# Kernel optimization log

Hardware: AMD Instinct MI355X
Metric: run time of the kernel (lower is better)

The kernel has to match this reference:

```python
import jax, jax.numpy as jnp
import numpy as np

C = 256          # channels
G = 4            # dcn groups
GC = C // G      # channels per group
K = 3            # dcn kernel size
P = K * K        # sampling points per group
OS = 0.5         # offset_scale
PAD = 1
N, H, W = 2, 128, 128


def setup_inputs() -> dict:
    key = jax.random.key(0)
    ks = jax.random.split(key, 8)
    f = lambda k, shp, s: jax.random.normal(k, shp, dtype=jnp.float32) * s
    return {
        "sampled_feat": jax.random.normal(ks[0], (N, H, W, C), dtype=jnp.float32),
        "context_info": jax.random.normal(ks[1], (N, H, W, C), dtype=jnp.float32),
        "W_in": f(ks[2], (C, C), 0.02),            # input_proj weight
        "b_in": jnp.zeros((C,), jnp.float32),
        "dw_kernel": f(ks[3], (3, 3, 1, C), 0.02),  # depthwise conv (HWIO, I=1)
        "dw_bias": jnp.zeros((C,), jnp.float32),
        "W_om": f(ks[4], (C, G * P * 3), 0.01),     # offset+mask projection
        "b_om": jnp.zeros((G * P * 3,), jnp.float32),
        "W_out": f(ks[5], (C, C), 0.02),            # output_proj (no bias)
        "ln_gamma": jnp.ones((C,), jnp.float32),
        "ln_beta": jnp.zeros((C,), jnp.float32),
    }


def _dcn_forward(sampled_feat, context_info, W_in, b_in, dw_kernel, dw_bias,
                 W_om, b_om, W_out, ln_gamma, ln_beta):
    Hp, Wp = H + 2 * PAD, W + 2 * PAD
    # value branch: pointwise input_proj then spatial zero-pad
    value = sampled_feat @ W_in + b_in
    value = jnp.pad(value, ((0, 0), (PAD, PAD), (PAD, PAD), (0, 0)))
    valg = value.reshape(N, Hp * Wp, G, GC).transpose(0, 2, 1, 3)  # (N,G,Hp*Wp,GC)

    # offset/mask branch (extra_offset_mask=True -> computed from context_info)
    ctx = jax.lax.conv_general_dilated(
        context_info, dw_kernel, (1, 1), ((1, 1), (1, 1)),
        dimension_numbers=("NHWC", "HWIO", "NHWC"), feature_group_count=C) + dw_bias
    om = (ctx @ W_om + b_om).reshape(N, H, W, G, 3 * P)
    offset = om[..., :2 * P].reshape(N, H, W, G, P, 2)  # (x,y) per sampling point
    mask = om[..., 2 * P:]                               # (N,H,W,G,P); DCNv4: no softmax

    # sampling locations in padded-input pixel coords (align_corners=False convention)
    kk = jnp.arange(K, dtype=jnp.float32) - (K - 1) // 2
    kx = jnp.tile(kk, K)      # (P,)
    ky = jnp.repeat(kk, K)    # (P,)
    base_x = (jnp.arange(W, dtype=jnp.float32) + PAD)[None, None, :, None, None]
    base_y = (jnp.arange(H, dtype=jnp.float32) + PAD)[None, :, None, None, None]
    px = base_x + OS * (kx + offset[..., 0])   # (N,H,W,G,P)
    py = base_y + OS * (ky + offset[..., 1])
    px = px.transpose(0, 3, 1, 2, 4).reshape(N, G, -1)  # (N,G,H*W*P)
    py = py.transpose(0, 3, 1, 2, 4).reshape(N, G, -1)

    # bilinear sampling with zero padding outside the padded input
    x0 = jnp.floor(px); y0 = jnp.floor(py)
    wx1 = px - x0; wy1 = py - y0

    def corner(xi, yi, w):
        valid = (xi >= 0) & (xi <= Wp - 1) & (yi >= 0) & (yi <= Hp - 1)
        idx = (jnp.clip(yi, 0, Hp - 1) * Wp + jnp.clip(xi, 0, Wp - 1)).astype(jnp.int32)
        v = jnp.take_along_axis(valg, idx[..., None], axis=2)  # (N,G,S,GC)
        return v * (w * valid)[..., None]

    samp = (corner(x0, y0, (1 - wx1) * (1 - wy1))
            + corner(x0 + 1, y0, wx1 * (1 - wy1))
            + corner(x0, y0 + 1, (1 - wx1) * wy1)
            + corner(x0 + 1, y0 + 1, wx1 * wy1))
    samp = samp.reshape(N, G, H, W, P, GC)
    maskg = mask.transpose(0, 3, 1, 2, 4)  # (N,G,H,W,P)
    out = jnp.einsum("nghwpc,nghwp->nhwgc", samp, maskg).reshape(N, H, W, C)

    out = out @ W_out  # output_proj, output_bias=False
    # LayerNorm over channels + exact GELU
    mu = out.mean(-1, keepdims=True)
    var = out.var(-1, keepdims=True)
    out = (out - mu) * jax.lax.rsqrt(var + 1e-5) * ln_gamma + ln_beta
    return jax.nn.gelu(out, approximate=False)


def reference(sampled_feat, context_info, W_in, b_in, dw_kernel, dw_bias,
              W_om, b_om, W_out, ln_gamma, ln_beta):
    return _dcn_forward(sampled_feat, context_info, W_in, b_in, dw_kernel, dw_bias,
                        W_om, b_om, W_out, ln_gamma, ln_beta)
```

## Files before the change

### kernel.cpp

```cpp
#include <hip/hip_runtime.h>
#include <math.h>

constexpr int NBATCH = 2, HH = 128, WW = 128, CC = 256, GC = 64;
constexpr int PP = 9, OMW = 108;
constexpr int MM = NBATCH * HH * WW;
constexpr int BTCOLS = 640;

using bf8 = __attribute__((ext_vector_type(8))) short;
using f32x4 = __attribute__((ext_vector_type(4))) float;

__device__ __forceinline__ short f2bf(float x) {
  unsigned u = __builtin_bit_cast(unsigned, x);
  unsigned r = (u + 0x7fffu + ((u >> 16) & 1u)) >> 16;
  return (short)r;
}
__device__ __forceinline__ float bf2f(short h) {
  unsigned u = ((unsigned)(unsigned short)h) << 16;
  return __builtin_bit_cast(float, u);
}

__global__ __launch_bounds__(256) void prep_kernel(
    const float* __restrict__ Win, const float* __restrict__ Wom,
    const float* __restrict__ Wout, short* __restrict__ Bh,
    short* __restrict__ Bl) {
  int gid = blockIdx.x * 256 + threadIdx.x;
  int col = gid >> 8, k = gid & 255;
  float w;
  if (col < 256)
    w = Win[k * 256 + col];
  else if (col < 384) {
    int c = col - 256;
    w = (c < OMW) ? Wom[k * OMW + c] : 0.f;
  } else {
    int c = col - 384;
    w = Wout[k * 256 + c];
  }
  short h = f2bf(w);
  short l = f2bf(w - bf2f(h));
  Bh[gid] = h;
  Bl[gid] = l;
}

__global__ __launch_bounds__(256) void dwconv_kernel(
    const float* __restrict__ x, const float* __restrict__ k,
    const float* __restrict__ b, float* __restrict__ y) {
  int gid = blockIdx.x * 256 + threadIdx.x;
  int q = gid & 63;
  int m = gid >> 6;
  int c = q * 4;
  int w = m & 127, h = (m >> 7) & 127, n = m >> 14;
  float4 acc = *(const float4*)&b[c];
#pragma unroll
  for (int dy = 0; dy < 3; ++dy) {
    int yy = h + dy - 1;
    if (yy < 0 || yy >= HH) continue;
#pragma unroll
    for (int dx = 0; dx < 3; ++dx) {
      int xx = w + dx - 1;
      if (xx < 0 || xx >= WW) continue;
      float4 v = *(const float4*)&x[(((size_t)n * HH + yy) * WW + xx) * CC + c];
      float4 kk = *(const float4*)&k[(dy * 3 + dx) * CC + c];
      acc.x += v.x * kk.x;
      acc.y += v.y * kk.y;
      acc.z += v.z * kk.z;
      acc.w += v.w * kk.w;
    }
  }
  *(float4*)&y[(size_t)m * CC + c] = acc;
}

template <int BN, int NOUT, bool BIAS, bool LN>
__global__ __launch_bounds__(BN == 256 ? 512 : 256) void mgemm(
    const float* __restrict__ A, const short* __restrict__ Bth,
    const short* __restrict__ Btl, const float* __restrict__ bias,
    float* __restrict__ Co, const float* __restrict__ lng,
    const float* __restrict__ lnb) {
  constexpr int BM = 128, BK = 32;
  constexpr int NT = (BN == 256) ? 512 : 256;
  constexpr int WN = BN / 64;
  __shared__ __align__(16) short Ah[BM][BK], Al[BM][BK];
  __shared__ __align__(16) short Bh[BN][BK], Bl[BN][BK];
  const int t = threadIdx.x;
  const int lane = t & 63, wid = t >> 6;
  const int wr = wid / WN, wc = wid % WN;
  const int l15 = lane & 15, l4 = lane >> 4;
  int mb, nb;
  if constexpr (BN == 128 && NOUT == 256) {
    mb = (int)(blockIdx.x >> 1) * BM;
    nb = (int)(blockIdx.x & 1) * 128;
  } else {
    mb = (int)blockIdx.x * BM;
    nb = 0;
  }

  f32x4 acc[4][4];
#pragma unroll
  for (int r = 0; r < 4; ++r)
#pragma unroll
    for (int n = 0; n < 4; ++n) acc[r][n] = (f32x4){0.f, 0.f, 0.f, 0.f};

  for (int ks = 0; ks < 256; ks += BK) {
#pragma unroll
    for (int i = 0; i < (BM * BK / 4) / NT; ++i) {
      int idx = t + NT * i;
      int row = idx >> 3, kq = idx & 7;
      float4 v = *(const float4*)&A[(size_t)(mb + row) * 256 + ks + kq * 4];
      short4 h = make_short4(f2bf(v.x), f2bf(v.y), f2bf(v.z), f2bf(v.w));
      short4 l =
          make_short4(f2bf(v.x - bf2f(h.x)), f2bf(v.y - bf2f(h.y)),
                      f2bf(v.z - bf2f(h.z)), f2bf(v.w - bf2f(h.w)));
      *(short4*)&Ah[row][kq * 4] = h;
      *(short4*)&Al[row][kq * 4] = l;
    }
#pragma unroll
    for (int i = 0; i < (BN * 4) / NT; ++i) {
      int idx = t + NT * i;
      int col = idx >> 2, q = idx & 3;
      *(bf8*)&Bh[col][q * 8] =
          *(const bf8*)&Bth[(size_t)(nb + col) * 256 + ks + q * 8];
      *(bf8*)&Bl[col][q * 8] =
          *(const bf8*)&Btl[(size_t)(nb + col) * 256 + ks + q * 8];
    }
    __syncthreads();

    bf8 ah[4], al[4], bh[4], bl[4];
#pragma unroll
    for (int r = 0; r < 4; ++r) {
      int row = wr * 64 + r * 16 + l15;
      ah[r] = *(const bf8*)&Ah[row][l4 * 8];
      al[r] = *(const bf8*)&Al[row][l4 * 8];
    }
#pragma unroll
    for (int n = 0; n < 4; ++n) {
      int col = wc * 64 + n * 16 + l15;
      bh[n] = *(const bf8*)&Bh[col][l4 * 8];
      bl[n] = *(const bf8*)&Bl[col][l4 * 8];
    }
#pragma unroll
    for (int r = 0; r < 4; ++r)
#pragma unroll
      for (int n = 0; n < 4; ++n) {
        acc[r][n] =
            __builtin_amdgcn_mfma_f32_16x16x32_bf16(al[r], bh[n], acc[r][n], 0, 0, 0);
        acc[r][n] =
            __builtin_amdgcn_mfma_f32_16x16x32_bf16(ah[r], bl[n], acc[r][n], 0, 0, 0);
        acc[r][n] =
            __builtin_amdgcn_mfma_f32_16x16x32_bf16(ah[r], bh[n], acc[r][n], 0, 0, 0);
      }
    __syncthreads();
  }

  if constexpr (LN) {
    __shared__ float red[BM][2];
    __shared__ float mu_s[BM], rs_s[BM];
    if (t < BM) {
      red[t][0] = 0.f;
      red[t][1] = 0.f;
    }
    __syncthreads();
#pragma unroll
    for (int r = 0; r < 4; ++r) {
#pragma unroll
      for (int reg = 0; reg < 4; ++reg) {
        float s = 0.f, ss = 0.f;
#pragma unroll
        for (int n = 0; n < 4; ++n) {
          float v = acc[r][n][reg];
          s += v;
          ss += v * v;
        }
#pragma unroll
        for (int m = 1; m < 16; m <<= 1) {
          s += __shfl_xor(s, m);
          ss += __shfl_xor(ss, m);
        }
        if (l15 == 0) {
          int row = wr * 64 + r * 16 + l4 * 4 + reg;
          atomicAdd(&red[row][0], s);
          atomicAdd(&red[row][1], ss);
        }
      }
    }
    __syncthreads();
    if (t < BM) {
      float mu = red[t][0] * (1.f / 256.f);
      float var = red[t][1] * (1.f / 256.f) - mu * mu;
      mu_s[t] = mu;
      rs_s[t] = rsqrtf(var + 1e-5f);
    }
    __syncthreads();
#pragma unroll
    for (int r = 0; r < 4; ++r)
#pragma unroll
      for (int reg = 0; reg < 4; ++reg) {
        int rloc = wr * 64 + r * 16 + l4 * 4 + reg;
        int row = mb + rloc;
        float mu = mu_s[rloc], rs = rs_s[rloc];
#pragma unroll
        for (int n = 0; n < 4; ++n) {
          int col = nb + wc * 64 + n * 16 + l15;
          float v = (acc[r][n][reg] - mu) * rs * lng[col] + lnb[col];
          Co[(size_t)row * NOUT + col] =
              0.5f * v * (1.f + erff(v * 0.70710678118654752f));
        }
      }
  } else {
#pragma unroll
    for (int r = 0; r < 4; ++r)
#pragma unroll
      for (int reg = 0; reg < 4; ++reg) {
        int row = mb + wr * 64 + r * 16 + l4 * 4 + reg;
#pragma unroll
        for (int n = 0; n < 4; ++n) {
          int col = nb + wc * 64 + n * 16 + l15;
          if (NOUT == BN * (256 / BN) || col < NOUT) {
            float v = acc[r][n][reg];
            if constexpr (BIAS) v += bias[col];
            if (col < NOUT) Co[(size_t)row * NOUT + col] = v;
          }
        }
      }
  }
}

__global__ __launch_bounds__(256) void sample_kernel(
    const float* __restrict__ val, const float* __restrict__ om,
    float* __restrict__ out) {
  int gid = blockIdx.x * 256 + threadIdx.x;
  int q = gid & 63;
  int m = gid >> 6;
  int g = q >> 4;
  int w = m & 127, h = (m >> 7) & 127, n = m >> 14;
  const float* omp = om + m * OMW + g * 27;
  const float* vb = val + (n << 22) + (q << 2);
  float bx = (float)(w + 1), by = (float)(h + 1);
  float4 acc = make_float4(0.f, 0.f, 0.f, 0.f);

#pragma unroll
  for (int p = 0; p < PP; ++p) {
    float px = bx + 0.5f * ((float)(p % 3 - 1) + omp[2 * p]);
    float py = by + 0.5f * ((float)(p / 3 - 1) + omp[2 * p + 1]);
    float mk = omp[18 + p];
    float x0f = floorf(px), y0f = floorf(py);
    int x0 = (int)x0f, y0 = (int)y0f;
    float wx1 = px - x0f, wy1 = py - y0f;
    float wx0 = 1.f - wx1, wy0 = 1.f - wy1;
    float4 s = make_float4(0.f, 0.f, 0.f, 0.f);
#define CORNER(XC, YC, WT)                                            \
  {                                                                   \
    int xc = (XC), yc = (YC);                                         \
    int xi = min(max(xc, 1), 128), yi = min(max(yc, 1), 128);         \
    float wt = ((xc == xi) && (yc == yi)) ? (WT) : 0.f;               \
    const float4 v =                                                  \
        *(const float4*)&vb[(((yi - 1) << 7) + (xi - 1)) << 8];       \
    s.x += v.x * wt;                                                  \
    s.y += v.y * wt;                                                  \
    s.z += v.z * wt;                                                  \
    s.w += v.w * wt;                                                  \
  }
    CORNER(x0, y0, wx0 * wy0);
    CORNER(x0 + 1, y0, wx1 * wy0);
    CORNER(x0, y0 + 1, wx0 * wy1);
    CORNER(x0 + 1, y0 + 1, wx1 * wy1);
#undef CORNER
    acc.x += mk * s.x;
    acc.y += mk * s.y;
    acc.z += mk * s.z;
    acc.w += mk * s.w;
  }
  *(float4*)&out[((size_t)m << 8) + (q << 2)] = acc;
}

extern "C" void kernel_launch(void* const* d_in, const int* in_sizes, int n_in,
                              void* d_out, int out_size, void* d_ws,
                              size_t ws_size, hipStream_t stream) {
  (void)in_sizes;
  (void)n_in;
  (void)out_size;
  (void)ws_size;
  const float* sampled = (const float*)d_in[0];
  const float* ctxin = (const float*)d_in[1];
  const float* W_in = (const float*)d_in[2];
  const float* b_in = (const float*)d_in[3];
  const float* dwk = (const float*)d_in[4];
  const float* dwb = (const float*)d_in[5];
  const float* W_om = (const float*)d_in[6];
  const float* b_om = (const float*)d_in[7];
  const float* W_out = (const float*)d_in[8];
  const float* lng = (const float*)d_in[9];
  const float* lnb = (const float*)d_in[10];
  float* out = (float*)d_out;

  float* ws = (float*)d_ws;
  float* value = ws;
  float* omb = value + (size_t)MM * CC;
  float* ctx_dcn = omb + (size_t)MM * OMW;
  short* Bth = (short*)(ctx_dcn + (size_t)MM * CC);
  short* Btl = Bth + (size_t)BTCOLS * 256;

  prep_kernel<<<BTCOLS, 256, 0, stream>>>(W_in, W_om, W_out, Bth, Btl);
  dwconv_kernel<<<MM * 64 / 256, 256, 0, stream>>>(ctxin, dwk, dwb, ctx_dcn);
  mgemm<128, 108, true, false><<<MM / 128, 256, 0, stream>>>(
      ctx_dcn, Bth + 256 * 256, Btl + 256 * 256, b_om, omb, nullptr, nullptr);
  mgemm<128, 256, true, false><<<2 * (MM / 128), 256, 0, stream>>>(
      sampled, Bth, Btl, b_in, value, nullptr, nullptr);
  sample_kernel<<<MM * 64 / 256, 256, 0, stream>>>(value, omb, ctx_dcn);
  mgemm<256, 256, false, true><<<MM / 128, 512, 0, stream>>>(
      ctx_dcn, Bth + 384 * 256, Btl + 384 * 256, nullptr, out, lng, lnb);
}
```

Measured before the change: 248.6 us.

## Pre-split activations to bf16 hi/lo and retile GEMMs with separate LN-GELU pass

Producers (dwconv, sample, and a new split kernel for the input features) now write bf16 hi/lo pairs directly, so the GEMM no longer converts fp32 A tiles inside its loop. The GEMM is retiled to 64x128 blocks with BK=64, padded shared-memory rows and an occupancy hint, and one kernel serves all three projections. The fused LayerNorm+GELU epilogue moves into a separate row-wise kernel, which adds an extra fp32 round trip through memory and two more launches.

Result: slower. 266.1 us (+7.1%).

```diff
diff --git a/kernel.cpp b/kernel.cpp
--- a/kernel.cpp
+++ b/kernel.cpp
@@ -1,7 +1,7 @@
 #include <hip/hip_runtime.h>
 #include <math.h>
 
-constexpr int NBATCH = 2, HH = 128, WW = 128, CC = 256, GC = 64;
+constexpr int NBATCH = 2, HH = 128, WW = 128, CC = 256;
 constexpr int PP = 9, OMW = 108;
 constexpr int MM = NBATCH * HH * WW;
 constexpr int BTCOLS = 640;
@@ -17,6 +17,12 @@
 __device__ __forceinline__ float bf2f(short h) {
   unsigned u = ((unsigned)(unsigned short)h) << 16;
   return __builtin_bit_cast(float, u);
+}
+__device__ __forceinline__ void split4(float4 v, short4* h, short4* l) {
+  short4 hh = make_short4(f2bf(v.x), f2bf(v.y), f2bf(v.z), f2bf(v.w));
+  *h = hh;
+  *l = make_short4(f2bf(v.x - bf2f(hh.x)), f2bf(v.y - bf2f(hh.y)),
+                   f2bf(v.z - bf2f(hh.z)), f2bf(v.w - bf2f(hh.w)));
 }
 
 __global__ __launch_bounds__(256) void prep_kernel(
@@ -36,14 +42,25 @@
     w = Wout[k * 256 + c];
   }
   short h = f2bf(w);
-  short l = f2bf(w - bf2f(h));
   Bh[gid] = h;
-  Bl[gid] = l;
+  Bl[gid] = f2bf(w - bf2f(h));
+}
+
+__global__ __launch_bounds__(256) void split_kernel(
+    const float* __restrict__ x, short* __restrict__ h,
+    short* __restrict__ l) {
+  int gid = blockIdx.x * 256 + threadIdx.x;
+  float4 v = *(const float4*)&x[(size_t)gid * 4];
+  short4 hh, ll;
+  split4(v, &hh, &ll);
+  *(short4*)&h[(size_t)gid * 4] = hh;
+  *(short4*)&l[(size_t)gid * 4] = ll;
 }
 
 __global__ __launch_bounds__(256) void dwconv_kernel(
     const float* __restrict__ x, const float* __restrict__ k,
-    const float* __restrict__ b, float* __restrict__ y) {
+    const float* __restrict__ b, short* __restrict__ yh,
+    short* __restrict__ yl) {
   int gid = blockIdx.x * 256 + threadIdx.x;
   int q = gid & 63;
   int m = gid >> 6;
@@ -66,166 +83,103 @@
       acc.w += v.w * kk.w;
     }
   }
-  *(float4*)&y[(size_t)m * CC + c] = acc;
-}
-
-template <int BN, int NOUT, bool BIAS, bool LN>
-__global__ __launch_bounds__(BN == 256 ? 512 : 256) void mgemm(
-    const float* __restrict__ A, const short* __restrict__ Bth,
-    const short* __restrict__ Btl, const float* __restrict__ bias,
-    float* __restrict__ Co, const float* __restrict__ lng,
-    const float* __restrict__ lnb) {
-  constexpr int BM = 128, BK = 32;
-  constexpr int NT = (BN == 256) ? 512 : 256;
-  constexpr int WN = BN / 64;
-  __shared__ __align__(16) short Ah[BM][BK], Al[BM][BK];
-  __shared__ __align__(16) short Bh[BN][BK], Bl[BN][BK];
+  short4 hh, ll;
+  split4(acc, &hh, &ll);
+  *(short4*)&yh[(size_t)m * CC + c] = hh;
+  *(short4*)&yl[(size_t)m * CC + c] = ll;
+}
+
+template <bool GUARD, bool BIAS>
+__global__ __launch_bounds__(256, 3) void mgemm(
+    const short* __restrict__ Ath, const short* __restrict__ Atl,
+    const short* __restrict__ Bth, const short* __restrict__ Btl,
+    const float* __restrict__ bias, float* __restrict__ Co, int nshift,
+    int nout) {
+  constexpr int BM = 64, BN = 128, BK = 64, SK = 68;
+  __shared__ __align__(16) short As[2][BM * SK];
+  __shared__ __align__(16) short Bs[2][BN * SK];
   const int t = threadIdx.x;
   const int lane = t & 63, wid = t >> 6;
-  const int wr = wid / WN, wc = wid % WN;
+  const int wr = wid >> 1, wc = wid & 1;
   const int l15 = lane & 15, l4 = lane >> 4;
-  int mb, nb;
-  if constexpr (BN == 128 && NOUT == 256) {
-    mb = (int)(blockIdx.x >> 1) * BM;
-    nb = (int)(blockIdx.x & 1) * 128;
-  } else {
-    mb = (int)blockIdx.x * BM;
-    nb = 0;
-  }
-
-  f32x4 acc[4][4];
-#pragma unroll
-  for (int r = 0; r < 4; ++r)
+  const int mb = ((int)blockIdx.x >> nshift) * BM;
+  const int nb = ((int)blockIdx.x & ((1 << nshift) - 1)) * BN;
+
+  f32x4 acc[2][4];
+#pragma unroll
+  for (int r = 0; r < 2; ++r)
 #pragma unroll
     for (int n = 0; n < 4; ++n) acc[r][n] = (f32x4){0.f, 0.f, 0.f, 0.f};
 
   for (int ks = 0; ks < 256; ks += BK) {
 #pragma unroll
-    for (int i = 0; i < (BM * BK / 4) / NT; ++i) {
-      int idx = t + NT * i;
-      int row = idx >> 3, kq = idx & 7;
-      float4 v = *(const float4*)&A[(size_t)(mb + row) * 256 + ks + kq * 4];
-      short4 h = make_short4(f2bf(v.x), f2bf(v.y), f2bf(v.z), f2bf(v.w));
-      short4 l =
-          make_short4(f2bf(v.x - bf2f(h.x)), f2bf(v.y - bf2f(h.y)),
-                      f2bf(v.z - bf2f(h.z)), f2bf(v.w - bf2f(h.w)));
-      *(short4*)&Ah[row][kq * 4] = h;
-      *(short4*)&Al[row][kq * 4] = l;
-    }
-#pragma unroll
-    for (int i = 0; i < (BN * 4) / NT; ++i) {
-      int idx = t + NT * i;
-      int col = idx >> 2, q = idx & 3;
-      *(bf8*)&Bh[col][q * 8] =
-          *(const bf8*)&Bth[(size_t)(nb + col) * 256 + ks + q * 8];
-      *(bf8*)&Bl[col][q * 8] =
-          *(const bf8*)&Btl[(size_t)(nb + col) * 256 + ks + q * 8];
+    for (int i = 0; i < 2; ++i) {
+      int idx = t + 256 * i;
+      int row = idx >> 3, kq = (idx & 7) * 8;
+      size_t g = (size_t)(mb + row) * 256 + ks + kq;
+      *(bf8*)&As[0][row * SK + kq] = *(const bf8*)&Ath[g];
+      *(bf8*)&As[1][row * SK + kq] = *(const bf8*)&Atl[g];
+    }
+#pragma unroll
+    for (int i = 0; i < 4; ++i) {
+      int idx = t + 256 * i;
+      int col = idx >> 3, kq = (idx & 7) * 8;
+      size_t g = (size_t)(nb + col) * 256 + ks + kq;
+      *(bf8*)&Bs[0][col * SK + kq] = *(const bf8*)&Bth[g];
+      *(bf8*)&Bs[1][col * SK + kq] = *(const bf8*)&Btl[g];
     }
     __syncthreads();
-
-    bf8 ah[4], al[4], bh[4], bl[4];
-#pragma unroll
-    for (int r = 0; r < 4; ++r) {
-      int row = wr * 64 + r * 16 + l15;
-      ah[r] = *(const bf8*)&Ah[row][l4 * 8];
-      al[r] = *(const bf8*)&Al[row][l4 * 8];
-    }
-#pragma unroll
-    for (int n = 0; n < 4; ++n) {
-      int col = wc * 64 + n * 16 + l15;
-      bh[n] = *(const bf8*)&Bh[col][l4 * 8];
-      bl[n] = *(const bf8*)&Bl[col][l4 * 8];
-    }
-#pragma unroll
-    for (int r = 0; r < 4; ++r)
+#pragma unroll
+    for (int kk = 0; kk < 2; ++kk) {
+      int ko = kk * 32 + l4 * 8;
+      bf8 ah[2], al[2], bh[4], bl[4];
+#pragma unroll
+      for (int r = 0; r < 2; ++r) {
+        int row = wr * 32 + r * 16 + l15;
+        ah[r] = *(const bf8*)&As[0][row * SK + ko];
+        al[r] = *(const bf8*)&As[1][row * SK + ko];
+      }
 #pragma unroll
       for (int n = 0; n < 4; ++n) {
-        acc[r][n] =
-            __builtin_amdgcn_mfma_f32_16x16x32_bf16(al[r], bh[n], acc[r][n], 0, 0, 0);
-        acc[r][n] =
-            __builtin_amdgcn_mfma_f32_16x16x32_bf16(ah[r], bl[n], acc[r][n], 0, 0, 0);
-        acc[r][n] =
-            __builtin_amdgcn_mfma_f32_16x16x32_bf16(ah[r], bh[n], acc[r][n], 0, 0, 0);
+        int col = wc * 64 + n * 16 + l15;
+        bh[n] = *(const bf8*)&Bs[0][col * SK + ko];
+        bl[n] = *(const bf8*)&Bs[1][col * SK + ko];
       }
+#pragma unroll
+      for (int r = 0; r < 2; ++r)
+#pragma unroll
+        for (int n = 0; n < 4; ++n) {
+          acc[r][n] = __builtin_amdgcn_mfma_f32_16x16x32_bf16(al[r], bh[n],
+                                                              acc[r][n], 0, 0, 0);
+          acc[r][n] = __builtin_amdgcn_mfma_f32_16x16x32_bf16(ah[r], bl[n],
+                                                              acc[r][n], 0, 0, 0);
+          acc[r][n] = __builtin_amdgcn_mfma_f32_16x16x32_bf16(ah[r], bh[n],
+                                                              acc[r][n], 0, 0, 0);
+        }
+    }
     __syncthreads();
   }
 
-  if constexpr (LN) {
-    __shared__ float red[BM][2];
-    __shared__ float mu_s[BM], rs_s[BM];
-    if (t < BM) {
-      red[t][0] = 0.f;
-      red[t][1] = 0.f;
-    }
-    __syncthreads();
-#pragma unroll
-    for (int r = 0; r < 4; ++r) {
-#pragma unroll
-      for (int reg = 0; reg < 4; ++reg) {
-        float s = 0.f, ss = 0.f;
-#pragma unroll
-        for (int n = 0; n < 4; ++n) {
+#pragma unroll
+  for (int r = 0; r < 2; ++r)
+#pragma unroll
+    for (int reg = 0; reg < 4; ++reg) {
+      int row = mb + wr * 32 + r * 16 + l4 * 4 + reg;
+#pragma unroll
+      for (int n = 0; n < 4; ++n) {
+        int col = nb + wc * 64 + n * 16 + l15;
+        if (!GUARD || col < nout) {
           float v = acc[r][n][reg];
-          s += v;
-          ss += v * v;
-        }
-#pragma unroll
-        for (int m = 1; m < 16; m <<= 1) {
-          s += __shfl_xor(s, m);
-          ss += __shfl_xor(ss, m);
-        }
-        if (l15 == 0) {
-          int row = wr * 64 + r * 16 + l4 * 4 + reg;
-          atomicAdd(&red[row][0], s);
-          atomicAdd(&red[row][1], ss);
+          if constexpr (BIAS) v += bias[col];
+          Co[(size_t)row * nout + col] = v;
         }
       }
     }
-    __syncthreads();
-    if (t < BM) {
-      float mu = red[t][0] * (1.f / 256.f);
-      float var = red[t][1] * (1.f / 256.f) - mu * mu;
-      mu_s[t] = mu;
-      rs_s[t] = rsqrtf(var + 1e-5f);
-    }
-    __syncthreads();
-#pragma unroll
-    for (int r = 0; r < 4; ++r)
-#pragma unroll
-      for (int reg = 0; reg < 4; ++reg) {
-        int rloc = wr * 64 + r * 16 + l4 * 4 + reg;
-        int row = mb + rloc;
-        float mu = mu_s[rloc], rs = rs_s[rloc];
-#pragma unroll
-        for (int n = 0; n < 4; ++n) {
-          int col = nb + wc * 64 + n * 16 + l15;
-          float v = (acc[r][n][reg] - mu) * rs * lng[col] + lnb[col];
-          Co[(size_t)row * NOUT + col] =
-              0.5f * v * (1.f + erff(v * 0.70710678118654752f));
-        }
-      }
-  } else {
-#pragma unroll
-    for (int r = 0; r < 4; ++r)
-#pragma unroll
-      for (int reg = 0; reg < 4; ++reg) {
-        int row = mb + wr * 64 + r * 16 + l4 * 4 + reg;
-#pragma unroll
-        for (int n = 0; n < 4; ++n) {
-          int col = nb + wc * 64 + n * 16 + l15;
-          if (NOUT == BN * (256 / BN) || col < NOUT) {
-            float v = acc[r][n][reg];
-            if constexpr (BIAS) v += bias[col];
-            if (col < NOUT) Co[(size_t)row * NOUT + col] = v;
-          }
-        }
-      }
-  }
 }
 
 __global__ __launch_bounds__(256) void sample_kernel(
     const float* __restrict__ val, const float* __restrict__ om,
-    float* __restrict__ out) {
+    short* __restrict__ oh, short* __restrict__ ol) {
   int gid = blockIdx.x * 256 + threadIdx.x;
   int q = gid & 63;
   int m = gid >> 6;
@@ -268,7 +222,40 @@
     acc.z += mk * s.z;
     acc.w += mk * s.w;
   }
-  *(float4*)&out[((size_t)m << 8) + (q << 2)] = acc;
+  short4 hh, ll;
+  split4(acc, &hh, &ll);
+  *(short4*)&oh[((size_t)m << 8) + (q << 2)] = hh;
+  *(short4*)&ol[((size_t)m << 8) + (q << 2)] = ll;
+}
+
+__global__ __launch_bounds__(256) void ln_gelu_kernel(
+    const float* __restrict__ x, const float* __restrict__ gam,
+    const float* __restrict__ bet, float* __restrict__ y) {
+  int row = blockIdx.x * 4 + (threadIdx.x >> 6);
+  int lane = threadIdx.x & 63;
+  const float* xr = x + (size_t)row * 256 + lane * 4;
+  float4 v = *(const float4*)xr;
+  float s = v.x + v.y + v.z + v.w;
+  float ss = v.x * v.x + v.y * v.y + v.z * v.z + v.w * v.w;
+#pragma unroll
+  for (int m = 1; m < 64; m <<= 1) {
+    s += __shfl_xor(s, m);
+    ss += __shfl_xor(ss, m);
+  }
+  float mu = s * (1.f / 256.f);
+  float var = ss * (1.f / 256.f) - mu * mu;
+  float rs = rsqrtf(var + 1e-5f);
+  float4 gg = *(const float4*)&gam[lane * 4];
+  float4 bb = *(const float4*)&bet[lane * 4];
+  float4 o;
+#define GEL(FIELD)                                                   \
+  {                                                                  \
+    float t_ = (v.FIELD - mu) * rs * gg.FIELD + bb.FIELD;            \
+    o.FIELD = 0.5f * t_ * (1.f + erff(t_ * 0.70710678118654752f));   \
+  }
+  GEL(x) GEL(y) GEL(z) GEL(w)
+#undef GEL
+  *(float4*)&y[(size_t)row * 256 + lane * 4] = o;
 }
 
 extern "C" void kernel_launch(void* const* d_in, const int* in_sizes, int n_in,
@@ -291,20 +278,28 @@
   const float* lnb = (const float*)d_in[10];
   float* out = (float*)d_out;
 
-  float* ws = (float*)d_ws;
-  float* value = ws;
+  float* value = (float*)d_ws;
   float* omb = value + (size_t)MM * CC;
-  float* ctx_dcn = omb + (size_t)MM * OMW;
-  short* Bth = (short*)(ctx_dcn + (size_t)MM * CC);
+  short* ctx_h = (short*)(omb + (size_t)MM * OMW);
+  short* ctx_l = ctx_h + (size_t)MM * CC;
+  short* xin_h = ctx_l + (size_t)MM * CC;
+  short* xin_l = xin_h + (size_t)MM * CC;
+  float* out_pre = (float*)(xin_l + (size_t)MM * CC);
+  short* Bth = (short*)(out_pre + (size_t)MM * CC);
   short* Btl = Bth + (size_t)BTCOLS * 256;
+  short* dcn_h = ctx_h;
+  short* dcn_l = ctx_l;
 
   prep_kernel<<<BTCOLS, 256, 0, stream>>>(W_in, W_om, W_out, Bth, Btl);
-  dwconv_kernel<<<MM * 64 / 256, 256, 0, stream>>>(ctxin, dwk, dwb, ctx_dcn);
-  mgemm<128, 108, true, false><<<MM / 128, 256, 0, stream>>>(
-      ctx_dcn, Bth + 256 * 256, Btl + 256 * 256, b_om, omb, nullptr, nullptr);
-  mgemm<128, 256, true, false><<<2 * (MM / 128), 256, 0, stream>>>(
-      sampled, Bth, Btl, b_in, value, nullptr, nullptr);
-  sample_kernel<<<MM * 64 / 256, 256, 0, stream>>>(value, omb, ctx_dcn);
-  mgemm<256, 256, false, true><<<MM / 128, 512, 0, stream>>>(
-      ctx_dcn, Bth + 384 * 256, Btl + 384 * 256, nullptr, out, lng, lnb);
-}
+  split_kernel<<<MM * 64 / 256, 256, 0, stream>>>(sampled, xin_h, xin_l);
+  dwconv_kernel<<<MM * 64 / 256, 256, 0, stream>>>(ctxin, dwk, dwb, ctx_h,
+                                                   ctx_l);
+  mgemm<true, true><<<MM / 64, 256, 0, stream>>>(
+      ctx_h, ctx_l, Bth + 256 * 256, Btl + 256 * 256, b_om, omb, 0, OMW);
+  mgemm<false, true><<<2 * (MM / 64), 256, 0, stream>>>(
+      xin_h, xin_l, Bth, Btl, b_in, value, 1, 256);
+  sample_kernel<<<MM * 64 / 256, 256, 0, stream>>>(value, omb, dcn_h, dcn_l);
+  mgemm<false, false><<<2 * (MM / 64), 256, 0, stream>>>(
+      dcn_h, dcn_l, Bth + 384 * 256, Btl + 384 * 256, nullptr, out_pre, 1, 256);
+  ln_gelu_kernel<<<MM / 4, 256, 0, stream>>>(out_pre, lng, lnb, out);
+}
```
